# Kernel optimization log

Measured on AMD Instinct MI355X. Metric: run time of the kernel, lower is better.

Reference implementation:

```python
import jax, jax.numpy as jnp
import numpy as np

HIDDEN = 2048
NUM_HEADS = 16
HEAD_DIM = HIDDEN // NUM_HEADS  # 128
SCALE = HEAD_DIM ** -0.5


def setup_inputs() -> dict:
    key = jax.random.key(0)
    ks = jax.random.split(key, 5)
    B, S = 2, 2048
    init = HIDDEN ** -0.5  # roughly kaiming-uniform scale for Linear weights
    return {
        "hidden_states": jax.random.normal(ks[0], (B, S, HIDDEN), dtype=jnp.float32),
        "Wq": jax.random.normal(ks[1], (HIDDEN, HIDDEN), dtype=jnp.float32) * init,
        "Wk": jax.random.normal(ks[2], (HIDDEN, HIDDEN), dtype=jnp.float32) * init,
        "Wv": jax.random.normal(ks[3], (HIDDEN, HIDDEN), dtype=jnp.float32) * init,
        "Wo": jax.random.normal(ks[4], (HIDDEN, HIDDEN), dtype=jnp.float32) * init,
    }


def reference(hidden_states, Wq, Wk, Wv, Wo):
    B, S, _ = hidden_states.shape
    # Projections (nn.Linear: x @ W.T; weights stored as [out, in])
    q = (hidden_states @ Wq.T).reshape(B, S, NUM_HEADS, HEAD_DIM).transpose(0, 2, 1, 3)
    k = (hidden_states @ Wk.T).reshape(B, S, NUM_HEADS, HEAD_DIM).transpose(0, 2, 1, 3)
    v = (hidden_states @ Wv.T).reshape(B, S, NUM_HEADS, HEAD_DIM).transpose(0, 2, 1, 3)
    # Full quadratic attention (faithful to the source's explicit materialization)
    scores = jnp.einsum("bhqd,bhkd->bhqk", q, k) * SCALE  # [B,H,S,S]
    probs = jax.nn.softmax(scores, axis=-1)
    attn = jnp.einsum("bhqk,bhkd->bhqd", probs, v)  # [B,H,S,Dh]
    attn = attn.transpose(0, 2, 1, 3).reshape(B, S, HIDDEN)
    return attn @ Wo.T
```

## Files before the change

### kernel.cpp

```cpp
#include <hip/hip_runtime.h>
#include <cstdint>

#define HIDDEN 2048
#define NHEADS 16
#define DH 128
#define BATCH 2
#define SEQ 2048
#define MTOT 4096
#define BH (BATCH * NHEADS)

typedef __attribute__((ext_vector_type(8))) short bf16x8;
typedef __attribute__((ext_vector_type(4))) float f32x4;

static constexpr float QSCALE = (float)(0.08838834764831845 * 1.4426950408889634);

__device__ __forceinline__ unsigned short f2bf(float f) {
  union { float f; uint32_t u; } v; v.f = f;
  uint32_t r = v.u + 0x7FFFu + ((v.u >> 16) & 1u);
  return (unsigned short)(r >> 16);
}
__device__ __forceinline__ uint32_t cvtpk(float lo, float hi) {
  uint32_t r;
  asm("v_cvt_pk_bf16_f32 %0, %1, %2" : "=v"(r) : "v"(lo), "v"(hi));
  return r;
}
__device__ __forceinline__ f32x4 mfma16(bf16x8 a, bf16x8 b, f32x4 c) {
  return __builtin_amdgcn_mfma_f32_16x16x32_bf16(a, b, c, 0, 0, 0);
}

typedef const __attribute__((address_space(1))) unsigned char* gas1_t;
typedef __attribute__((address_space(3))) unsigned char* las3_t;
__device__ __forceinline__ void gll16(const void* g, void* l) {
  __builtin_amdgcn_global_load_lds((gas1_t)g, (las3_t)l, 16, 0, 0);
}

template <int N>
__device__ __forceinline__ void waitvm() {
  if constexpr (N == 6) asm volatile("s_waitcnt vmcnt(6)" ::: "memory");
  else if constexpr (N == 0) asm volatile("s_waitcnt vmcnt(0)" ::: "memory");
}

__global__ __launch_bounds__(256) void cast_all(
    const float* __restrict__ X, const float* __restrict__ Wq,
    const float* __restrict__ Wk, const float* __restrict__ Wv,
    const float* __restrict__ Wo, unsigned short* __restrict__ Xb,
    unsigned short* __restrict__ Wqb, unsigned short* __restrict__ Wkb,
    unsigned short* __restrict__ Wvb, unsigned short* __restrict__ Wob) {
  const int n1 = MTOT * HIDDEN;
  const int i = (blockIdx.x * 256 + threadIdx.x) * 4;
  const float* s;
  unsigned short* d;
  int o;
  if (i < n1) {
    s = X; d = Xb; o = i;
  } else {
    const int j = i - n1;
    const int w = j >> 22;
    o = j & ((1 << 22) - 1);
    s = (w == 0) ? Wq : (w == 1) ? Wk : (w == 2) ? Wv : Wo;
    d = (w == 0) ? Wqb : (w == 1) ? Wkb : (w == 2) ? Wvb : Wob;
  }
  float4 f = *(const float4*)&s[o];
  ushort4 u;
  u.x = f2bf(f.x); u.y = f2bf(f.y); u.z = f2bf(f.z); u.w = f2bf(f.w);
  *(ushort4*)&d[o] = u;
}

template <int VM, bool PF>
__device__ __forceinline__ void pipe_body(
    int kt, char* SM, const unsigned short* aS0, const unsigned short* aS1,
    const unsigned short* bS0, const unsigned short* bS1,
    const unsigned short* bS2, const unsigned short* bS3, int wv, int wr,
    int wc, int g, int lr, f32x4 (&acc)[4][4]) {
  const char* Ac = SM + (kt % 3) * 49152;
  const char* Bc = Ac + 16384;
  char* slot2 = SM + ((kt + 2) % 3) * 49152;
  const size_t ko = (size_t)(kt + 2) * 64;
  const int rx = lr & 7;
  bf16x8 af[4], bfr[4];
#pragma unroll
  for (int mi = 0; mi < 4; ++mi)
    af[mi] = *(const bf16x8*)(Ac + (wr * 64 + mi * 16 + lr) * 128 + ((g ^ rx) * 16));
#pragma unroll
  for (int ni = 0; ni < 4; ++ni)
    bfr[ni] = *(const bf16x8*)(Bc + (wc * 64 + ni * 16 + lr) * 128 + ((g ^ rx) * 16));
  if (PF) {
    gll16(aS0 + ko, slot2 + wv * 2048);
    gll16(aS1 + ko, slot2 + wv * 2048 + 1024);
    gll16(bS0 + ko, slot2 + 16384 + wv * 4096);
  }
  __builtin_amdgcn_s_barrier();
  __builtin_amdgcn_s_setprio(1);
#pragma unroll
  for (int mi = 0; mi < 4; ++mi)
#pragma unroll
    for (int ni = 0; ni < 4; ++ni)
      acc[mi][ni] = mfma16(af[mi], bfr[ni], acc[mi][ni]);
  __builtin_amdgcn_s_setprio(0);
  __builtin_amdgcn_s_barrier();
#pragma unroll
  for (int mi = 0; mi < 4; ++mi)
    af[mi] = *(const bf16x8*)(Ac + (wr * 64 + mi * 16 + lr) * 128 + (((4 + g) ^ rx) * 16));
#pragma unroll
  for (int ni = 0; ni < 4; ++ni)
    bfr[ni] = *(const bf16x8*)(Bc + (wc * 64 + ni * 16 + lr) * 128 + (((4 + g) ^ rx) * 16));
  if (PF) {
    gll16(bS1 + ko, slot2 + 16384 + wv * 4096 + 1024);
    gll16(bS2 + ko, slot2 + 16384 + wv * 4096 + 2048);
    gll16(bS3 + ko, slot2 + 16384 + wv * 4096 + 3072);
  }
  __builtin_amdgcn_s_barrier();
  __builtin_amdgcn_s_setprio(1);
#pragma unroll
  for (int mi = 0; mi < 4; ++mi)
#pragma unroll
    for (int ni = 0; ni < 4; ++ni)
      acc[mi][ni] = mfma16(af[mi], bfr[ni], acc[mi][ni]);
  __builtin_amdgcn_s_setprio(0);
  if (VM >= 0) waitvm<VM>();
  __builtin_amdgcn_s_barrier();
}

#define PIPE_SETUP(Abase, Bbase)                                              \
  const int idxA0 = wv * 128 + lane, idxA1 = idxA0 + 64;                      \
  const int rA0 = idxA0 >> 3, cA0 = (idxA0 & 7) ^ (rA0 & 7);                  \
  const int rA1 = idxA1 >> 3, cA1 = (idxA1 & 7) ^ (rA1 & 7);                  \
  const unsigned short* aS0 = (Abase) + (size_t)(m0 + rA0) * HIDDEN + cA0 * 8;\
  const unsigned short* aS1 = (Abase) + (size_t)(m0 + rA1) * HIDDEN + cA1 * 8;\
  const int idxB0 = wv * 256 + lane, idxB1 = idxB0 + 64,                      \
            idxB2 = idxB0 + 128, idxB3 = idxB0 + 192;                         \
  const int rB0 = idxB0 >> 3, cB0 = (idxB0 & 7) ^ (rB0 & 7);                  \
  const int rB1 = idxB1 >> 3, cB1 = (idxB1 & 7) ^ (rB1 & 7);                  \
  const int rB2 = idxB2 >> 3, cB2 = (idxB2 & 7) ^ (rB2 & 7);                  \
  const int rB3 = idxB3 >> 3, cB3 = (idxB3 & 7) ^ (rB3 & 7);                  \
  const unsigned short* bS0 = (Bbase) + (size_t)(n0 + rB0) * HIDDEN + cB0 * 8;\
  const unsigned short* bS1 = (Bbase) + (size_t)(n0 + rB1) * HIDDEN + cB1 * 8;\
  const unsigned short* bS2 = (Bbase) + (size_t)(n0 + rB2) * HIDDEN + cB2 * 8;\
  const unsigned short* bS3 = (Bbase) + (size_t)(n0 + rB3) * HIDDEN + cB3 * 8;

#define PIPE_PROLOGUE()                                                       \
  _Pragma("unroll") for (int tt = 0; tt < 2; ++tt) {                          \
    char* slot = SM + tt * 49152;                                             \
    const size_t ko = (size_t)tt * 64;                                        \
    gll16(aS0 + ko, slot + wv * 2048);                                        \
    gll16(aS1 + ko, slot + wv * 2048 + 1024);                                 \
    gll16(bS0 + ko, slot + 16384 + wv * 4096);                                \
    gll16(bS1 + ko, slot + 16384 + wv * 4096 + 1024);                         \
    gll16(bS2 + ko, slot + 16384 + wv * 4096 + 2048);                         \
    gll16(bS3 + ko, slot + 16384 + wv * 4096 + 3072);                         \
  }                                                                           \
  waitvm<6>();                                                                \
  __builtin_amdgcn_s_barrier();

#define PIPE_LOOP()                                                           \
  for (int kt = 0; kt < 30; ++kt)                                             \
    pipe_body<6, true>(kt, SM, aS0, aS1, bS0, bS1, bS2, bS3, wv, wr, wc, g,   \
                       lr, acc);                                              \
  pipe_body<0, false>(30, SM, aS0, aS1, bS0, bS1, bS2, bS3, wv, wr, wc, g,    \
                      lr, acc);                                               \
  pipe_body<-1, false>(31, SM, aS0, aS1, bS0, bS1, bS2, bS3, wv, wr, wc, g,   \
                       lr, acc);

__global__ __launch_bounds__(512) void gemm_qkv_pipe(
    const unsigned short* __restrict__ A, const unsigned short* __restrict__ Wq,
    const unsigned short* __restrict__ Wk, const unsigned short* __restrict__ Wv,
    unsigned short* __restrict__ Qb, unsigned short* __restrict__ Kb,
    unsigned short* __restrict__ Vb) {
  __shared__ __align__(16) char SM[147456];
  const int tid = threadIdx.x;
  const int lane = tid & 63, wv = tid >> 6;
  const int wr = wv >> 2, wc = wv & 3;
  const int g = lane >> 4, lr = lane & 15;
  const int which = blockIdx.x >> 3;
  const int m0 = blockIdx.y * 128, n0 = (blockIdx.x & 7) * 256;
  const unsigned short* W = (which == 0) ? Wq : (which == 1) ? Wk : Wv;

  PIPE_SETUP(A, W)

  f32x4 acc[4][4];
#pragma unroll
  for (int i = 0; i < 4; ++i)
#pragma unroll
    for (int j = 0; j < 4; ++j) acc[i][j] = (f32x4){0.f, 0.f, 0.f, 0.f};

  PIPE_PROLOGUE()
  PIPE_LOOP()

  const float alpha = (which == 0) ? QSCALE : 1.0f;
  unsigned short* C = (which == 0) ? Qb : (which == 1) ? Kb : Vb;
#pragma unroll
  for (int mi = 0; mi < 4; ++mi)
#pragma unroll
    for (int ni = 0; ni < 4; ++ni)
#pragma unroll
      for (int r = 0; r < 4; ++r) {
        const int row = m0 + wr * 64 + mi * 16 + g * 4 + r;
        const int col = n0 + wc * 64 + ni * 16 + lr;
        const unsigned short v = f2bf(acc[mi][ni][r] * alpha);
        const int b = row >> 11, s = row & (SEQ - 1);
        const int h = col >> 7, d = col & (DH - 1);
        const size_t base = (size_t)(b * NHEADS + h) * SEQ * DH;
        if (which == 0)
          C[base + (size_t)s * DH + d] = v;
        else if (which == 1)
          C[base + (size_t)(s >> 5) * 4096 + (d >> 3) * 256 + (s & 31) * 8 + (d & 7)] = v;
        else
          C[base + (size_t)(s >> 3) * 1024 + d * 8 + (s & 7)] = v;
      }
}

__global__ __launch_bounds__(512) void gemm_out_pipe(
    const unsigned short* __restrict__ A, const unsigned short* __restrict__ W,
    float* __restrict__ C) {
  __shared__ __align__(16) char SM[147456];
  const int tid = threadIdx.x;
  const int lane = tid & 63, wv = tid >> 6;
  const int wr = wv >> 2, wc = wv & 3;
  const int g = lane >> 4, lr = lane & 15;
  const int m0 = blockIdx.y * 128, n0 = blockIdx.x * 256;

  PIPE_SETUP(A, W)

  f32x4 acc[4][4];
#pragma unroll
  for (int i = 0; i < 4; ++i)
#pragma unroll
    for (int j = 0; j < 4; ++j) acc[i][j] = (f32x4){0.f, 0.f, 0.f, 0.f};

  PIPE_PROLOGUE()
  PIPE_LOOP()

#pragma unroll
  for (int mi = 0; mi < 4; ++mi)
#pragma unroll
    for (int ni = 0; ni < 4; ++ni)
#pragma unroll
      for (int r = 0; r < 4; ++r) {
        const int row = m0 + wr * 64 + mi * 16 + g * 4 + r;
        const int col = n0 + wc * 64 + ni * 16 + lr;
        C[(size_t)row * HIDDEN + col] = acc[mi][ni][r];
      }
}

__global__ __launch_bounds__(256, 3) void attn_mfma(const unsigned short* __restrict__ Q,
                                                    const unsigned short* __restrict__ K,
                                                    const unsigned short* __restrict__ V,
                                                    unsigned short* __restrict__ Ab) {
  const int bid = blockIdx.x;
  const int bh = bid & 31;
  const int q0 = (bid >> 5) * 128;
  const int tid = threadIdx.x;
  const int wv = tid >> 6, lane = tid & 63;
  const int g = lane >> 4, lr = lane & 15;
  const unsigned short* Qh = Q + (size_t)bh * SEQ * DH;
  const unsigned short* Kh = K + (size_t)bh * SEQ * DH;
  const unsigned short* Vh = V + (size_t)bh * SEQ * DH;

  __shared__ __align__(16) unsigned short Kls[3][4096];
  __shared__ __align__(16) unsigned short Vls[3][4096];
  __shared__ __align__(16) unsigned short Pw[4][16][40];

  bf16x8 qf[2][4];
#pragma unroll
  for (int m = 0; m < 2; ++m)
#pragma unroll
    for (int kb = 0; kb < 4; ++kb)
      qf[m][kb] = *(const bf16x8*)&Qh[(size_t)(q0 + wv * 32 + m * 16 + lr) * DH +
                                      kb * 32 + g * 8];

  f32x4 acc[2][8];
#pragma unroll
  for (int m = 0; m < 2; ++m)
#pragma unroll
    for (int dn = 0; dn < 8; ++dn) acc[m][dn] = (f32x4){0.f, 0.f, 0.f, 0.f};
  float mrun[2] = {-1e30f, -1e30f};
  float lrun[2] = {0.f, 0.f};

#pragma unroll
  for (int tt = 0; tt < 2; ++tt)
#pragma unroll
    for (int j = 0; j < 2; ++j) {
      const int c = j * 256 + tid;
      gll16(Kh + (size_t)tt * 4096 + c * 8, (char*)&Kls[tt][0] + j * 4096 + wv * 1024);
      gll16(Vh + (size_t)tt * 4096 + c * 8, (char*)&Vls[tt][0] + j * 4096 + wv * 1024);
    }

  for (int t = 0; t < 64; ++t) {
    const int cur = t % 3;
    asm volatile("s_waitcnt vmcnt(4)" ::: "memory");
    __builtin_amdgcn_s_barrier();
    if (t + 2 < 64) {
      const int nx = (t + 2) % 3;
      const unsigned short* Kn = Kh + (size_t)(t + 2) * 4096;
      const unsigned short* Vn = Vh + (size_t)(t + 2) * 4096;
      char* kd = (char*)&Kls[nx][0];
      char* vd = (char*)&Vls[nx][0];
#pragma unroll
      for (int j = 0; j < 2; ++j) {
        const int c = j * 256 + tid;
        gll16(Kn + (size_t)c * 8, kd + j * 4096 + wv * 1024);
        gll16(Vn + (size_t)c * 8, vd + j * 4096 + wv * 1024);
      }
    }

    const char* Kc = (const char*)&Kls[cur][0];
    const char* Vc = (const char*)&Vls[cur][0];
    bf16x8 ap[2];
#pragma unroll
    for (int m = 0; m < 2; ++m) {
      f32x4 st0 = (f32x4){0.f, 0.f, 0.f, 0.f};
      f32x4 st1 = (f32x4){0.f, 0.f, 0.f, 0.f};
      __builtin_amdgcn_s_setprio(1);
#pragma unroll
      for (int kb = 0; kb < 4; ++kb) {
        const int cb = (kb * 4 + g) * 32;
        bf16x8 kf0 = *(const bf16x8*)(Kc + (cb + lr) * 16);
        bf16x8 kf1 = *(const bf16x8*)(Kc + (cb + 16 + lr) * 16);
        st0 = mfma16(kf0, qf[m][kb], st0);
        st1 = mfma16(kf1, qf[m][kb], st1);
      }
      __builtin_amdgcn_s_setprio(0);
      float mt = fmaxf(fmaxf(fmaxf(st0[0], st0[1]), fmaxf(st0[2], st0[3])),
                       fmaxf(fmaxf(st1[0], st1[1]), fmaxf(st1[2], st1[3])));
      mt = fmaxf(mt, __shfl_xor(mt, 16));
      mt = fmaxf(mt, __shfl_xor(mt, 32));
      if (!__all(mt <= mrun[m] + 8.0f)) {
        const float mnew = fmaxf(mrun[m], mt);
        const float corr = __builtin_amdgcn_exp2f(mrun[m] - mnew);
        lrun[m] *= corr;
        mrun[m] = mnew;
        const f32x4 cv = (f32x4){__shfl(corr, g * 4 + 0), __shfl(corr, g * 4 + 1),
                                 __shfl(corr, g * 4 + 2), __shfl(corr, g * 4 + 3)};
#pragma unroll
        for (int dn = 0; dn < 8; ++dn) acc[m][dn] *= cv;
      }
      float p[8], ls = 0.f;
#pragma unroll
      for (int r = 0; r < 4; ++r) {
        p[r] = __builtin_amdgcn_exp2f(st0[r] - mrun[m]);
        p[4 + r] = __builtin_amdgcn_exp2f(st1[r] - mrun[m]);
        ls += p[r] + p[4 + r];
      }
      lrun[m] += ls;
      uint2 pk0, pk1;
      pk0.x = cvtpk(p[0], p[1]); pk0.y = cvtpk(p[2], p[3]);
      pk1.x = cvtpk(p[4], p[5]); pk1.y = cvtpk(p[6], p[7]);
      *(uint2*)&Pw[wv][lr][4 * g] = pk0;
      *(uint2*)&Pw[wv][lr][16 + 4 * g] = pk1;
      ap[m] = *(const bf16x8*)&Pw[wv][lr][8 * g];
    }
    __builtin_amdgcn_s_setprio(1);
#pragma unroll
    for (int dn = 0; dn < 8; ++dn) {
      bf16x8 vf = *(const bf16x8*)(Vc + (g * 128 + dn * 16 + lr) * 16);
      acc[0][dn] = mfma16(ap[0], vf, acc[0][dn]);
      acc[1][dn] = mfma16(ap[1], vf, acc[1][dn]);
    }
    __builtin_amdgcn_s_setprio(0);
  }

  const int b = bh >> 4, h = bh & 15;
#pragma unroll
  for (int m = 0; m < 2; ++m) {
    lrun[m] += __shfl_xor(lrun[m], 16);
    lrun[m] += __shfl_xor(lrun[m], 32);
    const float inv = 1.f / lrun[m];
    float ir[4];
#pragma unroll
    for (int r = 0; r < 4; ++r) ir[r] = __shfl(inv, g * 4 + r);
#pragma unroll
    for (int dn = 0; dn < 8; ++dn)
#pragma unroll
      for (int r = 0; r < 4; ++r) {
        const int srow = q0 + wv * 32 + m * 16 + g * 4 + r;
        Ab[((size_t)(b * SEQ + srow) * NHEADS + h) * DH + dn * 16 + lr] =
            f2bf(acc[m][dn][r] * ir[r]);
      }
  }
}

extern "C" void kernel_launch(void* const* d_in, const int* in_sizes, int n_in,
                              void* d_out, int out_size, void* d_ws,
                              size_t ws_size, hipStream_t stream) {
  const float* X  = (const float*)d_in[0];
  const float* Wq = (const float*)d_in[1];
  const float* Wk = (const float*)d_in[2];
  const float* Wv = (const float*)d_in[3];
  const float* Wo = (const float*)d_in[4];
  float* out = (float*)d_out;

  const int n1 = MTOT * HIDDEN;
  const int n2 = HIDDEN * HIDDEN;

  char* p = (char*)d_ws;
  unsigned short* Xb  = (unsigned short*)(p + 0);
  unsigned short* Qb  = (unsigned short*)(p + 16777216);
  unsigned short* Kb  = (unsigned short*)(p + 33554432);
  unsigned short* Vb  = (unsigned short*)(p + 50331648);
  unsigned short* Wqb = (unsigned short*)(p + 67108864);
  unsigned short* Wkb = (unsigned short*)(p + 75497472);
  unsigned short* Wvb = (unsigned short*)(p + 83886080);
  unsigned short* Wob = (unsigned short*)(p + 92274688);
  unsigned short* Ab  = (unsigned short*)(p + 100663296);

  cast_all<<<(n1 + 4 * n2) / 1024, 256, 0, stream>>>(X, Wq, Wk, Wv, Wo, Xb, Wqb,
                                                     Wkb, Wvb, Wob);

  gemm_qkv_pipe<<<dim3(24, MTOT / 128), 512, 0, stream>>>(Xb, Wqb, Wkb, Wvb,
                                                          Qb, Kb, Vb);

  attn_mfma<<<dim3(512), 256, 0, stream>>>(Qb, Kb, Vb, Ab);

  gemm_out_pipe<<<dim3(HIDDEN / 256, MTOT / 128), 512, 0, stream>>>(Ab, Wob, out);
}
```

Measured before the change: 272.7 us.

## Enlarge GEMM tiles to 256x256 with double-buffered half-K LDS pipeline

Both projection GEMMs switch from 128x256 block tiles with a triple-buffered 64-wide K pipeline to 256x256 tiles. Each warp now holds an 8x4 accumulator grid, and LDS is double-buffered with split 32-wide K halves and a 4-way XOR swizzle. The larger tile raises arithmetic intensity and cuts global/LDS traffic per FLOP. The cost is fewer blocks: 384 for the QKV GEMM and 128 for the output GEMM, which may underfill the 256 CUs, plus more accumulator registers.

Result: slower. 311.4 us (+14.2%).

```diff
diff --git a/kernel.cpp b/kernel.cpp
--- a/kernel.cpp
+++ b/kernel.cpp
@@ -32,12 +32,6 @@
 typedef __attribute__((address_space(3))) unsigned char* las3_t;
 __device__ __forceinline__ void gll16(const void* g, void* l) {
   __builtin_amdgcn_global_load_lds((gas1_t)g, (las3_t)l, 16, 0, 0);
-}
-
-template <int N>
-__device__ __forceinline__ void waitvm() {
-  if constexpr (N == 6) asm volatile("s_waitcnt vmcnt(6)" ::: "memory");
-  else if constexpr (N == 0) asm volatile("s_waitcnt vmcnt(0)" ::: "memory");
 }
 
 __global__ __launch_bounds__(256) void cast_all(
@@ -66,28 +60,28 @@
   *(ushort4*)&d[o] = u;
 }
 
-template <int VM, bool PF>
-__device__ __forceinline__ void pipe_body(
-    int kt, char* SM, const unsigned short* aS0, const unsigned short* aS1,
-    const unsigned short* bS0, const unsigned short* bS1,
-    const unsigned short* bS2, const unsigned short* bS3, int wv, int wr,
-    int wc, int g, int lr, f32x4 (&acc)[4][4]) {
-  const char* Ac = SM + (kt % 3) * 49152;
-  const char* Bc = Ac + 16384;
-  char* slot2 = SM + ((kt + 2) % 3) * 49152;
-  const size_t ko = (size_t)(kt + 2) * 64;
-  const int rx = lr & 7;
-  bf16x8 af[4], bfr[4];
-#pragma unroll
-  for (int mi = 0; mi < 4; ++mi)
-    af[mi] = *(const bf16x8*)(Ac + (wr * 64 + mi * 16 + lr) * 128 + ((g ^ rx) * 16));
+template <int VM, bool PF1, bool PF2>
+__device__ __forceinline__ void tile_body(
+    int t, char* SM, const unsigned short* pa, const unsigned short* pb,
+    int wv, int wr, int wc, int g, int lr, f32x4 (&acc)[8][4]) {
+  char* buf  = SM + (size_t)((t & 1) * 65536);
+  char* obuf = SM + (size_t)(((t + 1) & 1) * 65536);
+  const int swz16 = (g ^ (lr & 3)) * 16;
+  const size_t ko1 = (size_t)(t + 1) * 64 + 32;
+  const size_t ko0 = (size_t)(t + 2) * 64;
+  const size_t rowskip = (size_t)128 * HIDDEN;
+  bf16x8 a[4], b[4];
+
+#pragma unroll
+  for (int mi = 0; mi < 4; ++mi)
+    a[mi] = *(const bf16x8*)(buf + (wr * 128 + mi * 16 + lr) * 64 + swz16);
 #pragma unroll
   for (int ni = 0; ni < 4; ++ni)
-    bfr[ni] = *(const bf16x8*)(Bc + (wc * 64 + ni * 16 + lr) * 128 + ((g ^ rx) * 16));
-  if (PF) {
-    gll16(aS0 + ko, slot2 + wv * 2048);
-    gll16(aS1 + ko, slot2 + wv * 2048 + 1024);
-    gll16(bS0 + ko, slot2 + 16384 + wv * 4096);
+    b[ni] = *(const bf16x8*)(buf + 32768 + (wc * 64 + ni * 16 + lr) * 64 + swz16);
+  if (PF1) {
+    char* d = obuf + 16384 + wv * 1024;
+    gll16(pa + ko1, d);
+    gll16(pa + rowskip + ko1, d + 8192);
   }
   __builtin_amdgcn_s_barrier();
   __builtin_amdgcn_s_setprio(1);
@@ -95,19 +89,38 @@
   for (int mi = 0; mi < 4; ++mi)
 #pragma unroll
     for (int ni = 0; ni < 4; ++ni)
-      acc[mi][ni] = mfma16(af[mi], bfr[ni], acc[mi][ni]);
+      acc[mi][ni] = mfma16(a[mi], b[ni], acc[mi][ni]);
   __builtin_amdgcn_s_setprio(0);
   __builtin_amdgcn_s_barrier();
-#pragma unroll
-  for (int mi = 0; mi < 4; ++mi)
-    af[mi] = *(const bf16x8*)(Ac + (wr * 64 + mi * 16 + lr) * 128 + (((4 + g) ^ rx) * 16));
+
+#pragma unroll
+  for (int mi = 0; mi < 4; ++mi)
+    a[mi] = *(const bf16x8*)(buf + (wr * 128 + 64 + mi * 16 + lr) * 64 + swz16);
+  if (PF1) {
+    char* d = obuf + 32768 + 16384 + wv * 1024;
+    gll16(pb + ko1, d);
+    gll16(pb + rowskip + ko1, d + 8192);
+  }
+  __builtin_amdgcn_s_barrier();
+  __builtin_amdgcn_s_setprio(1);
+#pragma unroll
+  for (int mi = 0; mi < 4; ++mi)
+#pragma unroll
+    for (int ni = 0; ni < 4; ++ni)
+      acc[4 + mi][ni] = mfma16(a[mi], b[ni], acc[4 + mi][ni]);
+  __builtin_amdgcn_s_setprio(0);
+  __builtin_amdgcn_s_barrier();
+
+#pragma unroll
+  for (int mi = 0; mi < 4; ++mi)
+    a[mi] = *(const bf16x8*)(buf + 16384 + (wr * 128 + mi * 16 + lr) * 64 + swz16);
 #pragma unroll
   for (int ni = 0; ni < 4; ++ni)
-    bfr[ni] = *(const bf16x8*)(Bc + (wc * 64 + ni * 16 + lr) * 128 + (((4 + g) ^ rx) * 16));
-  if (PF) {
-    gll16(bS1 + ko, slot2 + 16384 + wv * 4096 + 1024);
-    gll16(bS2 + ko, slot2 + 16384 + wv * 4096 + 2048);
-    gll16(bS3 + ko, slot2 + 16384 + wv * 4096 + 3072);
+    b[ni] = *(const bf16x8*)(buf + 32768 + 16384 + (wc * 64 + ni * 16 + lr) * 64 + swz16);
+  if (PF2) {
+    char* d = buf + wv * 1024;
+    gll16(pa + ko0, d);
+    gll16(pa + rowskip + ko0, d + 8192);
   }
   __builtin_amdgcn_s_barrier();
   __builtin_amdgcn_s_setprio(1);
@@ -115,86 +128,96 @@
   for (int mi = 0; mi < 4; ++mi)
 #pragma unroll
     for (int ni = 0; ni < 4; ++ni)
-      acc[mi][ni] = mfma16(af[mi], bfr[ni], acc[mi][ni]);
+      acc[mi][ni] = mfma16(a[mi], b[ni], acc[mi][ni]);
   __builtin_amdgcn_s_setprio(0);
-  if (VM >= 0) waitvm<VM>();
-  __builtin_amdgcn_s_barrier();
-}
-
-#define PIPE_SETUP(Abase, Bbase)                                              \
-  const int idxA0 = wv * 128 + lane, idxA1 = idxA0 + 64;                      \
-  const int rA0 = idxA0 >> 3, cA0 = (idxA0 & 7) ^ (rA0 & 7);                  \
-  const int rA1 = idxA1 >> 3, cA1 = (idxA1 & 7) ^ (rA1 & 7);                  \
-  const unsigned short* aS0 = (Abase) + (size_t)(m0 + rA0) * HIDDEN + cA0 * 8;\
-  const unsigned short* aS1 = (Abase) + (size_t)(m0 + rA1) * HIDDEN + cA1 * 8;\
-  const int idxB0 = wv * 256 + lane, idxB1 = idxB0 + 64,                      \
-            idxB2 = idxB0 + 128, idxB3 = idxB0 + 192;                         \
-  const int rB0 = idxB0 >> 3, cB0 = (idxB0 & 7) ^ (rB0 & 7);                  \
-  const int rB1 = idxB1 >> 3, cB1 = (idxB1 & 7) ^ (rB1 & 7);                  \
-  const int rB2 = idxB2 >> 3, cB2 = (idxB2 & 7) ^ (rB2 & 7);                  \
-  const int rB3 = idxB3 >> 3, cB3 = (idxB3 & 7) ^ (rB3 & 7);                  \
-  const unsigned short* bS0 = (Bbase) + (size_t)(n0 + rB0) * HIDDEN + cB0 * 8;\
-  const unsigned short* bS1 = (Bbase) + (size_t)(n0 + rB1) * HIDDEN + cB1 * 8;\
-  const unsigned short* bS2 = (Bbase) + (size_t)(n0 + rB2) * HIDDEN + cB2 * 8;\
-  const unsigned short* bS3 = (Bbase) + (size_t)(n0 + rB3) * HIDDEN + cB3 * 8;
-
-#define PIPE_PROLOGUE()                                                       \
-  _Pragma("unroll") for (int tt = 0; tt < 2; ++tt) {                          \
-    char* slot = SM + tt * 49152;                                             \
-    const size_t ko = (size_t)tt * 64;                                        \
-    gll16(aS0 + ko, slot + wv * 2048);                                        \
-    gll16(aS1 + ko, slot + wv * 2048 + 1024);                                 \
-    gll16(bS0 + ko, slot + 16384 + wv * 4096);                                \
-    gll16(bS1 + ko, slot + 16384 + wv * 4096 + 1024);                         \
-    gll16(bS2 + ko, slot + 16384 + wv * 4096 + 2048);                         \
-    gll16(bS3 + ko, slot + 16384 + wv * 4096 + 3072);                         \
+  __builtin_amdgcn_s_barrier();
+
+#pragma unroll
+  for (int mi = 0; mi < 4; ++mi)
+    a[mi] = *(const bf16x8*)(buf + 16384 + (wr * 128 + 64 + mi * 16 + lr) * 64 + swz16);
+  if (PF2) {
+    char* d = buf + 32768 + wv * 1024;
+    gll16(pb + ko0, d);
+    gll16(pb + rowskip + ko0, d + 8192);
+  }
+  __builtin_amdgcn_s_barrier();
+  __builtin_amdgcn_s_setprio(1);
+#pragma unroll
+  for (int mi = 0; mi < 4; ++mi)
+#pragma unroll
+    for (int ni = 0; ni < 4; ++ni)
+      acc[4 + mi][ni] = mfma16(a[mi], b[ni], acc[4 + mi][ni]);
+  __builtin_amdgcn_s_setprio(0);
+  if (VM == 4) asm volatile("s_waitcnt vmcnt(4)" ::: "memory");
+  else if (VM == 0) asm volatile("s_waitcnt vmcnt(0)" ::: "memory");
+  if (VM >= 0) __builtin_amdgcn_s_barrier();
+}
+
+#define PIPE256_SETUP(Abase, Bbase)                                           \
+  const int c0 = wv * 64 + lane;                                              \
+  const int row0 = c0 >> 2, j0 = (c0 & 3) ^ (row0 & 3);                       \
+  const unsigned short* pa = (Abase) + (size_t)(m0 + row0) * HIDDEN + j0 * 8; \
+  const unsigned short* pb = (Bbase) + (size_t)(n0 + row0) * HIDDEN + j0 * 8; \
+  const size_t rsk = (size_t)128 * HIDDEN;
+
+#define PIPE256_PROLOGUE()                                                    \
+  {                                                                           \
+    char* dA0 = SM + wv * 1024;                                               \
+    gll16(pa + 0, dA0); gll16(pa + rsk + 0, dA0 + 8192);                      \
+    char* dB0 = SM + 32768 + wv * 1024;                                       \
+    gll16(pb + 0, dB0); gll16(pb + rsk + 0, dB0 + 8192);                      \
+    char* dA1 = SM + 16384 + wv * 1024;                                       \
+    gll16(pa + 32, dA1); gll16(pa + rsk + 32, dA1 + 8192);                    \
+    char* dB1 = SM + 32768 + 16384 + wv * 1024;                               \
+    gll16(pb + 32, dB1); gll16(pb + rsk + 32, dB1 + 8192);                    \
+    char* eA0 = SM + 65536 + wv * 1024;                                       \
+    gll16(pa + 64, eA0); gll16(pa + rsk + 64, eA0 + 8192);                    \
+    char* eB0 = SM + 65536 + 32768 + wv * 1024;                               \
+    gll16(pb + 64, eB0); gll16(pb + rsk + 64, eB0 + 8192);                    \
   }                                                                           \
-  waitvm<6>();                                                                \
-  __builtin_amdgcn_s_barrier();
-
-#define PIPE_LOOP()                                                           \
-  for (int kt = 0; kt < 30; ++kt)                                             \
-    pipe_body<6, true>(kt, SM, aS0, aS1, bS0, bS1, bS2, bS3, wv, wr, wc, g,   \
-                       lr, acc);                                              \
-  pipe_body<0, false>(30, SM, aS0, aS1, bS0, bS1, bS2, bS3, wv, wr, wc, g,    \
-                      lr, acc);                                               \
-  pipe_body<-1, false>(31, SM, aS0, aS1, bS0, bS1, bS2, bS3, wv, wr, wc, g,   \
-                       lr, acc);
+  asm volatile("s_waitcnt vmcnt(4)" ::: "memory");                            \
+  __builtin_amdgcn_s_barrier();
+
+#define PIPE256_LOOP()                                                        \
+  for (int t = 0; t < 30; ++t)                                                \
+    tile_body<4, true, true>(t, SM, pa, pb, wv, wr, wc, g, lr, acc);          \
+  tile_body<0, true, false>(30, SM, pa, pb, wv, wr, wc, g, lr, acc);          \
+  tile_body<-1, false, false>(31, SM, pa, pb, wv, wr, wc, g, lr, acc);
 
 __global__ __launch_bounds__(512) void gemm_qkv_pipe(
     const unsigned short* __restrict__ A, const unsigned short* __restrict__ Wq,
     const unsigned short* __restrict__ Wk, const unsigned short* __restrict__ Wv,
     unsigned short* __restrict__ Qb, unsigned short* __restrict__ Kb,
     unsigned short* __restrict__ Vb) {
-  __shared__ __align__(16) char SM[147456];
+  __shared__ __align__(16) char SM[131072];
   const int tid = threadIdx.x;
   const int lane = tid & 63, wv = tid >> 6;
   const int wr = wv >> 2, wc = wv & 3;
   const int g = lane >> 4, lr = lane & 15;
   const int which = blockIdx.x >> 3;
-  const int m0 = blockIdx.y * 128, n0 = (blockIdx.x & 7) * 256;
+  const int m0 = blockIdx.y * 256, n0 = (blockIdx.x & 7) * 256;
   const unsigned short* W = (which == 0) ? Wq : (which == 1) ? Wk : Wv;
 
-  PIPE_SETUP(A, W)
-
-  f32x4 acc[4][4];
-#pragma unroll
-  for (int i = 0; i < 4; ++i)
+  PIPE256_SETUP(A, W)
+
+  f32x4 acc[8][4];
+#pragma unroll
+  for (int i = 0; i < 8; ++i)
 #pragma unroll
     for (int j = 0; j < 4; ++j) acc[i][j] = (f32x4){0.f, 0.f, 0.f, 0.f};
 
-  PIPE_PROLOGUE()
-  PIPE_LOOP()
+  PIPE256_PROLOGUE()
+  PIPE256_LOOP()
 
   const float alpha = (which == 0) ? QSCALE : 1.0f;
   unsigned short* C = (which == 0) ? Qb : (which == 1) ? Kb : Vb;
 #pragma unroll
-  for (int mi = 0; mi < 4; ++mi)
+  for (int mi = 0; mi < 8; ++mi)
 #pragma unroll
     for (int ni = 0; ni < 4; ++ni)
 #pragma unroll
       for (int r = 0; r < 4; ++r) {
-        const int row = m0 + wr * 64 + mi * 16 + g * 4 + r;
+        const int row = m0 + wr * 128 + mi * 16 + g * 4 + r;
         const int col = n0 + wc * 64 + ni * 16 + lr;
         const unsigned short v = f2bf(acc[mi][ni][r] * alpha);
         const int b = row >> 11, s = row & (SEQ - 1);
@@ -212,31 +235,31 @@
 __global__ __launch_bounds__(512) void gemm_out_pipe(
     const unsigned short* __restrict__ A, const unsigned short* __restrict__ W,
     float* __restrict__ C) {
-  __shared__ __align__(16) char SM[147456];
+  __shared__ __align__(16) char SM[131072];
   const int tid = threadIdx.x;
   const int lane = tid & 63, wv = tid >> 6;
   const int wr = wv >> 2, wc = wv & 3;
   const int g = lane >> 4, lr = lane & 15;
-  const int m0 = blockIdx.y * 128, n0 = blockIdx.x * 256;
-
-  PIPE_SETUP(A, W)
-
-  f32x4 acc[4][4];
-#pragma unroll
-  for (int i = 0; i < 4; ++i)
+  const int m0 = blockIdx.y * 256, n0 = blockIdx.x * 256;
+
+  PIPE256_SETUP(A, W)
+
+  f32x4 acc[8][4];
+#pragma unroll
+  for (int i = 0; i < 8; ++i)
 #pragma unroll
     for (int j = 0; j < 4; ++j) acc[i][j] = (f32x4){0.f, 0.f, 0.f, 0.f};
 
-  PIPE_PROLOGUE()
-  PIPE_LOOP()
-
-#pragma unroll
-  for (int mi = 0; mi < 4; ++mi)
+  PIPE256_PROLOGUE()
+  PIPE256_LOOP()
+
+#pragma unroll
+  for (int mi = 0; mi < 8; ++mi)
 #pragma unroll
     for (int ni = 0; ni < 4; ++ni)
 #pragma unroll
       for (int r = 0; r < 4; ++r) {
-        const int row = m0 + wr * 64 + mi * 16 + g * 4 + r;
+        const int row = m0 + wr * 128 + mi * 16 + g * 4 + r;
         const int col = n0 + wc * 64 + ni * 16 + lr;
         C[(size_t)row * HIDDEN + col] = acc[mi][ni][r];
       }
@@ -406,10 +429,10 @@
   cast_all<<<(n1 + 4 * n2) / 1024, 256, 0, stream>>>(X, Wq, Wk, Wv, Wo, Xb, Wqb,
                                                      Wkb, Wvb, Wob);
 
-  gemm_qkv_pipe<<<dim3(24, MTOT / 128), 512, 0, stream>>>(Xb, Wqb, Wkb, Wvb,
-                                                          Qb, Kb, Vb);
+  gemm_qkv_pipe<<<dim3(24, 16), 512, 0, stream>>>(Xb, Wqb, Wkb, Wvb,
+                                                  Qb, Kb, Vb);
 
   attn_mfma<<<dim3(512), 256, 0, stream>>>(Qb, Kb, Vb, Ab);
 
-  gemm_out_pipe<<<dim3(HIDDEN / 256, MTOT / 128), 512, 0, stream>>>(Ab, Wob, out);
-}
+  gemm_out_pipe<<<dim3(8, 16), 512, 0, stream>>>(Ab, Wob, out);
+}
```
